# Optimization experiments

Measured on AMD Instinct MI355X. Metric: run time of the kernel, lower is better.

The kernel has to match this reference:

```python
import jax, jax.numpy as jnp
import numpy as np

NUM_CLASSES = 10


def _decode(out, thresh, anchors, stride):
    # out: [B, 45, H, W] -> [B, H, W, 3, 15]
    B, C, H, W = out.shape
    o = out.transpose(0, 2, 3, 1).reshape(B, H, W, 3, -1)
    mask = o[..., 0] > thresh                      # [B,H,W,3]
    ys = jnp.arange(H, dtype=o.dtype)[None, :, None, None]
    xs = jnp.arange(W, dtype=o.dtype)[None, None, :, None]
    pre_x = (xs + o[..., 1]) * stride
    pre_y = (ys + o[..., 2]) * stride
    iou = o[..., 0]
    kind = jnp.argmax(o[..., 5:5 + NUM_CLASSES], axis=-1).astype(o.dtype)
    pre_w = anchors[:, 0] * jnp.exp(o[..., 3])     # anchors broadcast over last (anchor) dim
    pre_h = anchors[:, 1] * jnp.exp(o[..., 4])
    x1 = pre_x - 0.5 * pre_w
    y1 = pre_y - 0.5 * pre_h
    x2 = pre_x + 0.5 * pre_w
    y2 = pre_y + 0.5 * pre_h
    boxes = jnp.stack([iou, x1, y1, x2, y2, kind], axis=-1)  # [B,H,W,3,6]
    return boxes.reshape(-1, 6), mask.reshape(-1)


def setup_inputs() -> dict:
    key = jax.random.key(0)
    k = jax.random.split(key, 6)
    return {
        "output13": jax.random.normal(k[0], (128, 45, 13, 13), dtype=jnp.float32),
        "output26": jax.random.normal(k[1], (128, 45, 26, 26), dtype=jnp.float32),
        "output52": jax.random.normal(k[2], (128, 45, 52, 52), dtype=jnp.float32),
        "anchors13": jax.random.uniform(k[3], (3, 2), dtype=jnp.float32),
        "anchors26": jax.random.uniform(k[4], (3, 2), dtype=jnp.float32),
        "anchors52": jax.random.uniform(k[5], (3, 2), dtype=jnp.float32),
        "thresh": jnp.zeros((), dtype=jnp.float32),
    }


def reference(output13, output26, output52, anchors13, anchors26, anchors52, thresh):
    # JIT-friendly dense equivalent of mask -> nonzero -> gather -> decode:
    # decode every (batch, cell, anchor) slot and return the compaction mask
    # alongside; the masked rows correspond exactly to torch's gathered rows.
    b13, m13 = _decode(output13, thresh, anchors13, 32.0)
    b26, m26 = _decode(output26, thresh, anchors26, 16.0)
    b52, m52 = _decode(output52, thresh, anchors52, 8.0)
    boxes = jnp.concatenate([b13, b26, b52], axis=0)  # [N_total, 6]
    mask = jnp.concatenate([m13, m26, m52], axis=0)   # [N_total]
    return boxes, mask
```

## Files before the change

### kernel.cpp

```cpp
#include <hip/hip_runtime.h>


constexpr int  BATCH = 128;
constexpr long N13 = 128L * 13 * 13 * 3;
constexpr long N26 = 128L * 26 * 26 * 3;
constexpr long N52 = 128L * 52 * 52 * 3;
constexpr long NTOT = N13 + N26 + N52;

template <int H, int STRIDE, long ROWOFF>
__global__ __launch_bounds__(256) void decode_scale(
    const float* __restrict__ o,
    const float* __restrict__ anc,
    const float* __restrict__ threshp,
    float* __restrict__ out)
{
    const long N = (long)BATCH * H * H * 3;
    long rel = (long)blockIdx.x * blockDim.x + threadIdx.x;
    if (rel >= N) return;

    const float thresh = *threshp;

    int a = (int)(rel % 3);
    long cell = rel / 3;
    int x = (int)(cell % H);
    long t = cell / H;
    int y = (int)(t % H);
    int b = (int)(t / H);

    const long hw = (long)H * H;
    const float* p = o + (long)(b * 45 + a * 15) * hw + (long)y * H + x;

    float v[15];
#pragma unroll
    for (int j = 0; j < 15; ++j) v[j] = p[j * hw];

    float iou = v[0];
    float px = ((float)x + v[1]) * (float)STRIDE;
    float py = ((float)y + v[2]) * (float)STRIDE;
    float pw = anc[2 * a + 0] * expf(v[3]);
    float ph = anc[2 * a + 1] * expf(v[4]);

    int kind = 0;
    float best = v[5];
#pragma unroll
    for (int c = 1; c < 10; ++c) {
        if (v[5 + c] > best) { best = v[5 + c]; kind = c; }
    }

    long row = ROWOFF + rel;
    float2* orow = (float2*)out + row * 3;
    orow[0] = make_float2(iou, px - 0.5f * pw);
    orow[1] = make_float2(py - 0.5f * ph, px + 0.5f * pw);
    orow[2] = make_float2(py + 0.5f * ph, (float)kind);

    out[6 * NTOT + row] = (iou > thresh) ? 1.0f : 0.0f;
}

extern "C" void kernel_launch(void* const* d_in, const int* in_sizes, int n_in,
                              void* d_out, int out_size, void* d_ws, size_t ws_size,
                              hipStream_t stream) {
    const float* o13 = (const float*)d_in[0];
    const float* o26 = (const float*)d_in[1];
    const float* o52 = (const float*)d_in[2];
    const float* a13 = (const float*)d_in[3];
    const float* a26 = (const float*)d_in[4];
    const float* a52 = (const float*)d_in[5];
    const float* thr = (const float*)d_in[6];
    float* out = (float*)d_out;

    const int block = 256;
    decode_scale<13, 32, 0L>
        <<<(N13 + block - 1) / block, block, 0, stream>>>(o13, a13, thr, out);
    decode_scale<26, 16, N13>
        <<<(N26 + block - 1) / block, block, 0, stream>>>(o26, a26, thr, out);
    decode_scale<52, 8, N13 + N26>
        <<<(N52 + block - 1) / block, block, 0, stream>>>(o52, a52, thr, out);
}
```

Baseline: 135.5 us.

## Fuse three scale launches into one kernel with float4 vectorized loads

Replaces three per-scale kernel launches with a single launch that dispatches blocks to the 52, 26 and 13 scales by block index. For the two larger scales each thread now reads float4 chunks covering four adjacent cells per channel, so global loads are wider. The goal is to cut launch overhead and the number of load instructions. In exchange the output writes per thread become strided across four rows, which may reduce store coalescing, and each thread holds more registers.

```diff
diff --git a/kernel.cpp b/kernel.cpp
--- a/kernel.cpp
+++ b/kernel.cpp
@@ -7,28 +7,88 @@
 constexpr long N52 = 128L * 52 * 52 * 3;
 constexpr long NTOT = N13 + N26 + N52;
 
+constexpr int BLOCK = 256;
+constexpr int T52 = 128 * 3 * (52 * 52 / 4);
+constexpr int T26 = 128 * 3 * (26 * 26 / 4);
+constexpr int T13 = (int)N13;
+constexpr int B52 = (T52 + BLOCK - 1) / BLOCK;
+constexpr int B26 = (T26 + BLOCK - 1) / BLOCK;
+constexpr int B13 = (T13 + BLOCK - 1) / BLOCK;
+
 template <int H, int STRIDE, long ROWOFF>
-__global__ __launch_bounds__(256) void decode_scale(
-    const float* __restrict__ o,
-    const float* __restrict__ anc,
-    const float* __restrict__ threshp,
-    float* __restrict__ out)
+__device__ __forceinline__ void decode_vec(const float* __restrict__ o,
+                                           const float* __restrict__ anc,
+                                           float thresh,
+                                           float* __restrict__ out, int tid)
 {
-    const long N = (long)BATCH * H * H * 3;
-    long rel = (long)blockIdx.x * blockDim.x + threadIdx.x;
-    if (rel >= N) return;
+    constexpr int hw = H * H;
+    constexpr int C4 = hw / 4;
+    constexpr int NT = BATCH * 3 * C4;
+    if (tid >= NT) return;
 
-    const float thresh = *threshp;
+    int a = tid % 3;
+    int t = tid / 3;
+    int chunk = t % C4;
+    int b = t / C4;
 
-    int a = (int)(rel % 3);
-    long cell = rel / 3;
-    int x = (int)(cell % H);
-    long t = cell / H;
-    int y = (int)(t % H);
-    int b = (int)(t / H);
+    const float4* base = (const float4*)o + (b * 45 + a * 15) * C4 + chunk;
 
-    const long hw = (long)H * H;
-    const float* p = o + (long)(b * 45 + a * 15) * hw + (long)y * H + x;
+    float v[15][4];
+#pragma unroll
+    for (int j = 0; j < 15; ++j) {
+        float4 q = base[j * C4];
+        v[j][0] = q.x; v[j][1] = q.y; v[j][2] = q.z; v[j][3] = q.w;
+    }
+
+    float2 A = ((const float2*)anc)[a];
+
+    int cell0 = chunk * 4;
+    int x = cell0 % H;
+    int y = cell0 / H;
+    long row = ROWOFF + ((long)b * hw + cell0) * 3 + a;
+
+#pragma unroll
+    for (int i = 0; i < 4; ++i) {
+        float iou = v[0][i];
+        float px = ((float)x + v[1][i]) * (float)STRIDE;
+        float py = ((float)y + v[2][i]) * (float)STRIDE;
+        float pw = A.x * expf(v[3][i]);
+        float ph = A.y * expf(v[4][i]);
+
+        int kind = 0;
+        float best = v[5][i];
+#pragma unroll
+        for (int c = 1; c < 10; ++c)
+            if (v[5 + c][i] > best) { best = v[5 + c][i]; kind = c; }
+
+        float2* orow = (float2*)out + row * 3;
+        orow[0] = make_float2(iou, px - 0.5f * pw);
+        orow[1] = make_float2(py - 0.5f * ph, px + 0.5f * pw);
+        orow[2] = make_float2(py + 0.5f * ph, (float)kind);
+        out[6 * NTOT + row] = (iou > thresh) ? 1.0f : 0.0f;
+
+        row += 3;
+        if (++x == H) { x = 0; ++y; }
+    }
+}
+
+template <int H, int STRIDE, long ROWOFF>
+__device__ __forceinline__ void decode_scalar(const float* __restrict__ o,
+                                              const float* __restrict__ anc,
+                                              float thresh,
+                                              float* __restrict__ out, int tid)
+{
+    constexpr int hw = H * H;
+    constexpr int NT = BATCH * hw * 3;
+    if (tid >= NT) return;
+
+    int a = tid % 3;
+    int cell = tid / 3;
+    int x = (cell % hw) % H;
+    int y = (cell % hw) / H;
+    int b = cell / hw;
+
+    const float* p = o + (b * 45 + a * 15) * hw + y * H + x;
 
     float v[15];
 #pragma unroll
@@ -37,23 +97,39 @@
     float iou = v[0];
     float px = ((float)x + v[1]) * (float)STRIDE;
     float py = ((float)y + v[2]) * (float)STRIDE;
-    float pw = anc[2 * a + 0] * expf(v[3]);
-    float ph = anc[2 * a + 1] * expf(v[4]);
+    float2 A = ((const float2*)anc)[a];
+    float pw = A.x * expf(v[3]);
+    float ph = A.y * expf(v[4]);
 
     int kind = 0;
     float best = v[5];
 #pragma unroll
-    for (int c = 1; c < 10; ++c) {
+    for (int c = 1; c < 10; ++c)
         if (v[5 + c] > best) { best = v[5 + c]; kind = c; }
-    }
 
-    long row = ROWOFF + rel;
+    long row = ROWOFF + tid;
     float2* orow = (float2*)out + row * 3;
     orow[0] = make_float2(iou, px - 0.5f * pw);
     orow[1] = make_float2(py - 0.5f * ph, px + 0.5f * pw);
     orow[2] = make_float2(py + 0.5f * ph, (float)kind);
+    out[6 * NTOT + row] = (iou > thresh) ? 1.0f : 0.0f;
+}
 
-    out[6 * NTOT + row] = (iou > thresh) ? 1.0f : 0.0f;
+__global__ __launch_bounds__(256) void decode_all(
+    const float* __restrict__ o13, const float* __restrict__ o26,
+    const float* __restrict__ o52, const float* __restrict__ a13,
+    const float* __restrict__ a26, const float* __restrict__ a52,
+    const float* __restrict__ thr, float* __restrict__ out)
+{
+    const float thresh = *thr;
+    int blk = blockIdx.x;
+    if (blk < B52) {
+        decode_vec<52, 8, N13 + N26>(o52, a52, thresh, out, blk * BLOCK + (int)threadIdx.x);
+    } else if (blk < B52 + B26) {
+        decode_vec<26, 16, N13>(o26, a26, thresh, out, (blk - B52) * BLOCK + (int)threadIdx.x);
+    } else {
+        decode_scalar<13, 32, 0L>(o13, a13, thresh, out, (blk - B52 - B26) * BLOCK + (int)threadIdx.x);
+    }
 }
 
 extern "C" void kernel_launch(void* const* d_in, const int* in_sizes, int n_in,
@@ -68,11 +144,5 @@
     const float* thr = (const float*)d_in[6];
     float* out = (float*)d_out;
 
-    const int block = 256;
-    decode_scale<13, 32, 0L>
-        <<<(N13 + block - 1) / block, block, 0, stream>>>(o13, a13, thr, out);
-    decode_scale<26, 16, N13>
-        <<<(N26 + block - 1) / block, block, 0, stream>>>(o26, a26, thr, out);
-    decode_scale<52, 8, N13 + N26>
-        <<<(N52 + block - 1) / block, block, 0, stream>>>(o52, a52, thr, out);
+    decode_all<<<B52 + B26 + B13, BLOCK, 0, stream>>>(o13, o26, o52, a13, a26, a52, thr, out);
 }
```

Result: no change. 137.0 us (+1.1%).
